# Performance work log

Measured on AMD Instinct MI355X. Metric: run time of the kernel, lower is better.

Reference implementation:

```python
import jax, jax.numpy as jnp
import numpy as np

EMBED_DIM = 1024
NUM_HEADS = 16
HEAD_DIM = EMBED_DIM // NUM_HEADS


def setup_inputs() -> dict:
    key = jax.random.key(0)
    ks = jax.random.split(key, 11)
    B, L, E = 4, 1024, EMBED_DIM
    s = E ** -0.5  # xavier-ish init scale
    return {
        "query": jax.random.normal(ks[0], (B, L, E), dtype=jnp.float32),
        "key": jax.random.normal(ks[1], (B, L, E), dtype=jnp.float32),
        "value": jax.random.normal(ks[2], (B, L, E), dtype=jnp.float32),
        "Wq": jax.random.normal(ks[3], (E, E), dtype=jnp.float32) * s,
        "bq": jnp.zeros((E,), dtype=jnp.float32),
        "Wk": jax.random.normal(ks[4], (E, E), dtype=jnp.float32) * s,
        "bk": jnp.zeros((E,), dtype=jnp.float32),
        "Wv": jax.random.normal(ks[5], (E, E), dtype=jnp.float32) * s,
        "bv": jnp.zeros((E,), dtype=jnp.float32),
        "Wo": jax.random.normal(ks[6], (E, E), dtype=jnp.float32) * s,
        "bo": jnp.zeros((E,), dtype=jnp.float32),
    }


def reference(query, key, value, Wq, bq, Wk, bk, Wv, bv, Wo, bo):
    # torch nn.MultiheadAttention (batch_first=True), need_weights=True,
    # average_attn_weights=False, eval mode (dropout inactive), no masks,
    # followed by the wrapper's extra softmax on the returned weights.
    B, Lq, E = query.shape
    Lk = key.shape[1]
    H, Dh = NUM_HEADS, HEAD_DIM
    scale = Dh ** -0.5

    # projections -> [B, H, L, Dh]
    q = (query @ Wq.T + bq).reshape(B, Lq, H, Dh).transpose(0, 2, 1, 3) * scale
    k = (key @ Wk.T + bk).reshape(B, Lk, H, Dh).transpose(0, 2, 1, 3)
    v = (value @ Wv.T + bv).reshape(B, Lk, H, Dh).transpose(0, 2, 1, 3)

    scores = jnp.einsum("bhqd,bhkd->bhqk", q, k)      # [B, H, Lq, Lk]
    attn = jax.nn.softmax(scores, axis=-1)             # attention weights

    ctx = jnp.einsum("bhqk,bhkd->bhqd", attn, v)       # [B, H, Lq, Dh]
    ctx = ctx.transpose(0, 2, 1, 3).reshape(B, Lq, E)
    out = ctx @ Wo.T + bo                              # [B, Lq, E]

    weights = jax.nn.softmax(attn, axis=-1)            # wrapper's redundant softmax
    return (out, weights)
```

## Files before the change

### kernel.cpp

```cpp
#include <hip/hip_runtime.h>
#include <cstdint>
#include <cstddef>

typedef short bf16x8 __attribute__((ext_vector_type(8)));
typedef float f32x4 __attribute__((ext_vector_type(4)));
typedef int v4i __attribute__((ext_vector_type(4)));
typedef unsigned short u16;

#define DEVFN static __device__ __forceinline__

#define M2 11.5415603f

DEVFN u16 f2bf(float f) {
  uint32_t u = __float_as_uint(f);
  u += 0x7FFFu + ((u >> 16) & 1u);
  return (u16)(u >> 16);
}

DEVFN f32x4 mfma16(bf16x8 a, bf16x8 b, f32x4 c) {
  return __builtin_amdgcn_mfma_f32_16x16x32_bf16(a, b, c, 0, 0, 0);
}

struct CvtArgs {
  const float* src[7];
  u16* dst[7];
  int n4[7];
};

__global__ __launch_bounds__(256) void cvt_all(CvtArgs a) {
  const int w = blockIdx.y;
  const int n4 = a.n4[w];
  const float4* s = (const float4*)a.src[w];
  uint2* d = (uint2*)a.dst[w];
  for (int i = blockIdx.x * 256 + threadIdx.x; i < n4; i += gridDim.x * 256) {
    const float4 v = s[i];
    d[i] = make_uint2((uint32_t)f2bf(v.x) | ((uint32_t)f2bf(v.y) << 16),
                      (uint32_t)f2bf(v.z) | ((uint32_t)f2bf(v.w) << 16));
  }
}

struct ProjArgs {
  const u16* A[3];
  const u16* W[3];
  const float* bias[3];
  u16* C[3];
  float scale[3];
};

__global__ __launch_bounds__(256) void gemm_proj(ProjArgs P) {
  constexpr int KD = 1024;
  constexpr int ND = 1024;
  __shared__ __align__(16) u16 As[128 * 32];
  __shared__ __align__(16) u16 Bs[128 * 32];
  const int hw = blockIdx.x + 32 * (blockIdx.y + 8 * blockIdx.z);
  const int lb = (hw & 7) * 96 + (hw >> 3);
  const int bn = lb & 7;
  const int bm = (lb >> 3) & 31;
  const int z  = lb >> 8;
  const u16* __restrict__ A = P.A[z];
  const u16* __restrict__ W = P.W[z];
  const float* __restrict__ bias = P.bias[z];
  u16* __restrict__ C = P.C[z];
  const float scale = P.scale[z];

  const int tid = threadIdx.x;
  const int wave = tid >> 6, lane = tid & 63;
  const int wm = wave >> 1, wn = wave & 1;
  const int l16 = lane & 15, lg = lane >> 4;

  f32x4 acc[4][4] = {};
  const int ar = wave * 16 + (lane >> 2);
  const int ac = (lane & 3) * 8;

  for (int k0 = 0; k0 < KD; k0 += 32) {
#pragma unroll
    for (int half = 0; half < 2; half++) {
      const int r = ar + half * 64;
      const u16* ga = A + (size_t)(bm * 128 + r) * KD + k0 + ac;
      const u16* gb = W + (size_t)(bn * 128 + r) * KD + k0 + ac;
      __builtin_amdgcn_global_load_lds(
          (const __attribute__((address_space(1))) void*)ga,
          (__attribute__((address_space(3))) void*)(As + wave * 512 + half * 2048),
          16, 0, 0);
      __builtin_amdgcn_global_load_lds(
          (const __attribute__((address_space(1))) void*)gb,
          (__attribute__((address_space(3))) void*)(Bs + wave * 512 + half * 2048),
          16, 0, 0);
    }
    __syncthreads();
    bf16x8 af[4], bfv[4];
#pragma unroll
    for (int m = 0; m < 4; m++)
      af[m] = *(const bf16x8*)(&As[(wm * 64 + m * 16 + l16) * 32 + lg * 8]);
#pragma unroll
    for (int n = 0; n < 4; n++)
      bfv[n] = *(const bf16x8*)(&Bs[(wn * 64 + n * 16 + l16) * 32 + lg * 8]);
#pragma unroll
    for (int m = 0; m < 4; m++)
#pragma unroll
      for (int n = 0; n < 4; n++)
        acc[m][n] = mfma16(af[m], bfv[n], acc[m][n]);
    __syncthreads();
  }

  if (z == 2) {
#pragma unroll
    for (int m = 0; m < 4; m++) {
#pragma unroll
      for (int n = 0; n < 4; n++) {
        const int col = bn * 128 + wn * 64 + n * 16 + l16;
        const float bv = bias[col];
        const int hh = col >> 6, dd = col & 63;
        const int row0 = bm * 128 + wm * 64 + m * 16 + lg * 4;
        const int bb = row0 >> 10, ll = row0 & 1023;
        u16 tmp[4];
#pragma unroll
        for (int r = 0; r < 4; r++) tmp[r] = f2bf((acc[m][n][r] + bv) * scale);
        *(uint2*)(C + ((size_t)((bb * 16 + hh) * 64 + dd)) * 1024 + ll) =
            *(const uint2*)tmp;
      }
    }
  } else {
#pragma unroll
    for (int m = 0; m < 4; m++) {
#pragma unroll
      for (int n = 0; n < 4; n++) {
        const int col = bn * 128 + wn * 64 + n * 16 + l16;
        const float bv = bias[col];
#pragma unroll
        for (int r = 0; r < 4; r++) {
          const int row = bm * 128 + wm * 64 + m * 16 + lg * 4 + r;
          C[(size_t)row * ND + col] = f2bf((acc[m][n][r] + bv) * scale);
        }
      }
    }
  }
}

__global__ __launch_bounds__(256) void gemm_out(const u16* __restrict__ A,
                                                const u16* __restrict__ W,
                                                const float* __restrict__ bias,
                                                float* __restrict__ C) {
  constexpr int KD = 1024;
  constexpr int ND = 1024;
  __shared__ __align__(16) u16 As[128 * 32];
  __shared__ __align__(16) u16 Bs[64 * 32];
  const int hw = blockIdx.x + 32 * blockIdx.y;
  const int lb = (hw & 7) * 64 + (hw >> 3);
  const int bn = lb & 15;
  const int bm = lb >> 4;
  const int tid = threadIdx.x;
  const int wave = tid >> 6, lane = tid & 63;
  const int wm = wave >> 1, wn = wave & 1;
  const int l16 = lane & 15, lg = lane >> 4;

  f32x4 acc[4][2] = {};
  const int ar = wave * 16 + (lane >> 2);
  const int ac = (lane & 3) * 8;

  for (int k0 = 0; k0 < KD; k0 += 32) {
#pragma unroll
    for (int half = 0; half < 2; half++) {
      const u16* ga = A + (size_t)(bm * 128 + ar + half * 64) * KD + k0 + ac;
      __builtin_amdgcn_global_load_lds(
          (const __attribute__((address_space(1))) void*)ga,
          (__attribute__((address_space(3))) void*)(As + wave * 512 + half * 2048),
          16, 0, 0);
    }
    {
      const u16* gb = W + (size_t)(bn * 64 + ar) * KD + k0 + ac;
      __builtin_amdgcn_global_load_lds(
          (const __attribute__((address_space(1))) void*)gb,
          (__attribute__((address_space(3))) void*)(Bs + wave * 512),
          16, 0, 0);
    }
    __syncthreads();
    bf16x8 af[4], bfv[2];
#pragma unroll
    for (int m = 0; m < 4; m++)
      af[m] = *(const bf16x8*)(&As[(wm * 64 + m * 16 + l16) * 32 + lg * 8]);
#pragma unroll
    for (int n = 0; n < 2; n++)
      bfv[n] = *(const bf16x8*)(&Bs[(wn * 32 + n * 16 + l16) * 32 + lg * 8]);
#pragma unroll
    for (int m = 0; m < 4; m++)
#pragma unroll
      for (int n = 0; n < 2; n++)
        acc[m][n] = mfma16(af[m], bfv[n], acc[m][n]);
    __syncthreads();
  }

#pragma unroll
  for (int m = 0; m < 4; m++) {
#pragma unroll
    for (int n = 0; n < 2; n++) {
      const int col = bn * 64 + wn * 32 + n * 16 + l16;
      const float bv = bias[col];
#pragma unroll
      for (int r = 0; r < 4; r++) {
        const int row = bm * 128 + wm * 64 + m * 16 + lg * 4 + r;
        C[(size_t)row * ND + col] = acc[m][n][r] + bv;
      }
    }
  }
}

__global__ __launch_bounds__(512, 4) void flash_kernel(
    const u16* __restrict__ Qs, const u16* __restrict__ Kb,
    const u16* __restrict__ Vt, u16* __restrict__ Ctx,
    float* __restrict__ Wout) {
  __shared__ __align__(16) u16 Ks[128 * 72];
  __shared__ __align__(16) u16 Vs[64 * 136];
  __shared__ __align__(16) u16 Ps[8][16 * 136];
  const int hw = blockIdx.x + 8 * (blockIdx.y + 16 * blockIdx.z);
  const int lb = (hw & 7) * 64 + (hw >> 3);
  const int qt = lb & 7;
  const int h  = (lb >> 3) & 15;
  const int b  = lb >> 7;
  const int tid = threadIdx.x, wave = tid >> 6, lane = tid & 63;
  const int l16 = lane & 15, lg = lane >> 4;
  const int bh = b * 16 + h;
  const int qbase = qt * 128 + wave * 16;

  const u16* qp = Qs + ((size_t)(b * 1024 + qbase + l16)) * 1024 + h * 64 + lg * 8;
  const bf16x8 qa0 = *(const bf16x8*)qp;
  const bf16x8 qa1 = *(const bf16x8*)(qp + 32);

  const int krow = tid >> 3, kcol = (tid & 7) * 8;
  const int vrow = tid >> 3, vcol = (tid & 7) * 16;
  const u16* kgb = Kb + ((size_t)(b * 1024 + krow)) * 1024 + h * 64 + kcol;
  const u16* vgb = Vt + ((size_t)(bh * 64 + vrow)) * 1024 + vcol;
  u16* kds = &Ks[krow * 72 + kcol];
  u16* vds = &Vs[vrow * 136 + vcol];

  v4i kpre[2], vpre[2];
#define LOADK(K0)                                                         \
  {                                                                       \
    _Pragma("unroll") for (int i_ = 0; i_ < 2; i_++)                      \
        kpre[i_] = *(const v4i*)(kgb + ((size_t)(K0) + i_ * 64) * 1024);  \
  }
#define LOADV(K0)                                                         \
  {                                                                       \
    _Pragma("unroll") for (int i_ = 0; i_ < 2; i_++)                      \
        vpre[i_] = *(const v4i*)(vgb + (size_t)(K0) + i_ * 8);            \
  }
#define WRITEK                                                            \
  {                                                                       \
    _Pragma("unroll") for (int i_ = 0; i_ < 2; i_++)                      \
        *(v4i*)(kds + i_ * 64 * 72) = kpre[i_];                           \
  }
#define WRITEV                                                            \
  {                                                                       \
    _Pragma("unroll") for (int i_ = 0; i_ < 2; i_++)                      \
        *(v4i*)(vds + i_ * 8) = vpre[i_];                                 \
  }

  float lsum[4] = {}, m2[4] = {};
  f32x4 o[4] = {};

  LOADK(0) LOADV(0)
  WRITEK WRITEV
  __syncthreads();

  for (int t = 0; t < 8; t++) {
    if (t < 7) { LOADK((t + 1) * 128) LOADV((t + 1) * 128) }

    u16* pw = &Ps[wave][0];
#pragma unroll
    for (int j = 0; j < 8; j++) {
      const u16* kr = &Ks[(j * 16 + l16) * 72 + lg * 8];
      const bf16x8 kf0 = *(const bf16x8*)kr;
      const bf16x8 kf1 = *(const bf16x8*)(kr + 32);
      f32x4 z = {0.f, 0.f, 0.f, 0.f};
      z = mfma16(qa0, kf0, z);
      z = mfma16(qa1, kf1, z);
#pragma unroll
      for (int r = 0; r < 4; r++) {
        const float p = __builtin_amdgcn_exp2f(z[r] - M2);
        lsum[r] += p;
        m2[r] += p * p;
        pw[(lg * 4 + r) * 136 + j * 16 + l16] = f2bf(p);
      }
    }

    bf16x8 pa[4];
#pragma unroll
    for (int ks = 0; ks < 4; ks++)
      pa[ks] = *(const bf16x8*)(&pw[l16 * 136 + ks * 32 + lg * 8]);
#pragma unroll
    for (int ds = 0; ds < 4; ds++) {
#pragma unroll
      for (int ks = 0; ks < 4; ks++) {
        const bf16x8 vb = *(const bf16x8*)(&Vs[(ds * 16 + l16) * 136 + ks * 32 + lg * 8]);
        o[ds] = mfma16(pa[ks], vb, o[ds]);
      }
    }
    __syncthreads();
    if (t < 7) { WRITEK WRITEV __syncthreads(); }
  }

  LOADK(0)

#pragma unroll
  for (int r = 0; r < 4; r++) {
#pragma unroll
    for (int sft = 1; sft < 16; sft <<= 1) {
      lsum[r] += __shfl_xor(lsum[r], sft);
      m2[r] += __shfl_xor(m2[r], sft);
    }
  }

  float il_[4], inv2_[4];
#pragma unroll
  for (int r = 0; r < 4; r++) {
    const float il = 1.0f / lsum[r];
    il_[r] = il;
    const float s2 = 1025.0f + 0.5f * m2[r] * il * il;
    inv2_[r] = 1.0f / s2;
    const int qg = qbase + lg * 4 + r;
#pragma unroll
    for (int ds = 0; ds < 4; ds++)
      Ctx[((size_t)(b * 1024 + qg)) * 1024 + h * 64 + ds * 16 + l16] =
          f2bf(o[ds][r] * il);
  }

  float* wr = Wout + ((size_t)bh * 1024 + qbase + lg * 4) * 1024 + l16;
#define EMIT_TILE(K0)                                                     \
  {                                                                       \
    _Pragma("unroll") for (int j = 0; j < 8; j++) {                       \
      const u16* kr = &Ks[(j * 16 + l16) * 72 + lg * 8];                  \
      const bf16x8 kf0 = *(const bf16x8*)kr;                              \
      const bf16x8 kf1 = *(const bf16x8*)(kr + 32);                       \
      f32x4 z = {0.f, 0.f, 0.f, 0.f};                                     \
      z = mfma16(qa0, kf0, z);                                            \
      z = mfma16(qa1, kf1, z);                                            \
      _Pragma("unroll") for (int r = 0; r < 4; r++) {                     \
        const float a = __builtin_amdgcn_exp2f(z[r] - M2) * il_[r];       \
        float u = fmaf(a, 0.16666667f, 0.5f);                             \
        u = fmaf(a, u, 1.0f);                                             \
        u = fmaf(a, u, 1.0f);                                             \
        wr[(size_t)r * 1024 + (K0) + j * 16] = u * inv2_[r];              \
      }                                                                   \
    }                                                                     \
  }

  EMIT_TILE(896)
  __syncthreads();
  WRITEK
  __syncthreads();
  for (int t = 0; t < 7; t++) {
    if (t < 6) LOADK((t + 1) * 128)
    EMIT_TILE(t * 128)
    __syncthreads();
    if (t < 6) { WRITEK __syncthreads(); }
  }
#undef EMIT_TILE
#undef LOADK
#undef LOADV
#undef WRITEK
#undef WRITEV
}

extern "C" void kernel_launch(void* const* d_in, const int* in_sizes, int n_in,
                              void* d_out, int out_size, void* d_ws, size_t ws_size,
                              hipStream_t stream) {
  (void)in_sizes; (void)n_in; (void)out_size; (void)ws_size;
  const float* query = (const float*)d_in[0];
  const float* key   = (const float*)d_in[1];
  const float* value = (const float*)d_in[2];
  const float* Wq = (const float*)d_in[3];
  const float* bq = (const float*)d_in[4];
  const float* Wk = (const float*)d_in[5];
  const float* bk = (const float*)d_in[6];
  const float* Wv = (const float*)d_in[7];
  const float* bv = (const float*)d_in[8];
  const float* Wo = (const float*)d_in[9];
  const float* bo = (const float*)d_in[10];

  const size_t MB = 1ull << 20;
  char* w = (char*)d_ws;
  u16* xq  = (u16*)(w + 0 * MB);
  u16* xk  = (u16*)(w + 8 * MB);
  u16* xv  = (u16*)(w + 16 * MB);
  u16* wqb = (u16*)(w + 24 * MB);
  u16* wkb = (u16*)(w + 26 * MB);
  u16* wvb = (u16*)(w + 28 * MB);
  u16* wob = (u16*)(w + 30 * MB);
  u16* Qp  = (u16*)(w + 32 * MB);
  u16* Kp  = (u16*)(w + 40 * MB);
  u16* ctx = xq;

  float* Out = (float*)d_out;
  float* Wts = (float*)d_out + 4 * 1024 * 1024;
  u16* vt = (u16*)d_out;

  CvtArgs ca;
  ca.src[0] = query; ca.dst[0] = xq;  ca.n4[0] = 1048576;
  ca.src[1] = key;   ca.dst[1] = xk;  ca.n4[1] = 1048576;
  ca.src[2] = value; ca.dst[2] = xv;  ca.n4[2] = 1048576;
  ca.src[3] = Wq;    ca.dst[3] = wqb; ca.n4[3] = 262144;
  ca.src[4] = Wk;    ca.dst[4] = wkb; ca.n4[4] = 262144;
  ca.src[5] = Wv;    ca.dst[5] = wvb; ca.n4[5] = 262144;
  ca.src[6] = Wo;    ca.dst[6] = wob; ca.n4[6] = 262144;
  cvt_all<<<dim3(512, 7), 256, 0, stream>>>(ca);

  ProjArgs pa;
  pa.A[0] = xq; pa.W[0] = wqb; pa.bias[0] = bq; pa.C[0] = Qp;
  pa.scale[0] = 0.125f * 1.44269504f;
  pa.A[1] = xk; pa.W[1] = wkb; pa.bias[1] = bk; pa.C[1] = Kp; pa.scale[1] = 1.0f;
  pa.A[2] = xv; pa.W[2] = wvb; pa.bias[2] = bv; pa.C[2] = vt; pa.scale[2] = 1.0f;
  gemm_proj<<<dim3(32, 8, 3), 256, 0, stream>>>(pa);

  flash_kernel<<<dim3(8, 16, 4), 512, 0, stream>>>(Qp, Kp, vt, ctx, Wts);

  gemm_out<<<dim3(32, 16), 256, 0, stream>>>(ctx, wob, bo, Out);
}
```

Measured before the change: 171.2 us.

## Double K-tile depth in projection GEMM and XOR-swizzle LDS layout

The QKV projection GEMM now stages 64-wide K slices per iteration instead of 32, which halves the number of barrier pairs and loop iterations. Global-to-LDS copies place each 16-byte chunk at an XOR-swizzled column, and the fragment reads apply the matching swizzle, so LDS bank conflicts on the MFMA operand reads should drop. LDS use per block doubles, which may reduce occupancy, and the loop is still single-buffered with no overlap between loads and MFMAs.

```diff
diff --git a/kernel.cpp b/kernel.cpp
--- a/kernel.cpp
+++ b/kernel.cpp
@@ -50,8 +50,8 @@
 __global__ __launch_bounds__(256) void gemm_proj(ProjArgs P) {
   constexpr int KD = 1024;
   constexpr int ND = 1024;
-  __shared__ __align__(16) u16 As[128 * 32];
-  __shared__ __align__(16) u16 Bs[128 * 32];
+  __shared__ __align__(16) u16 As[128 * 64];
+  __shared__ __align__(16) u16 Bs[128 * 64];
   const int hw = blockIdx.x + 32 * (blockIdx.y + 8 * blockIdx.z);
   const int lb = (hw & 7) * 96 + (hw >> 3);
   const int bn = lb & 7;
@@ -69,37 +69,49 @@
   const int l16 = lane & 15, lg = lane >> 4;
 
   f32x4 acc[4][4] = {};
-  const int ar = wave * 16 + (lane >> 2);
-  const int ac = (lane & 3) * 8;
-
-  for (int k0 = 0; k0 < KD; k0 += 32) {
-#pragma unroll
-    for (int half = 0; half < 2; half++) {
-      const int r = ar + half * 64;
-      const u16* ga = A + (size_t)(bm * 128 + r) * KD + k0 + ac;
-      const u16* gb = W + (size_t)(bn * 128 + r) * KD + k0 + ac;
+  const int sr = wave * 8 + (lane >> 3);
+  const int scol = (((lane & 7) ^ (lane >> 3)) * 8);
+
+  for (int k0 = 0; k0 < KD; k0 += 64) {
+#pragma unroll
+    for (int q = 0; q < 4; q++) {
+      const int r = sr + q * 32;
+      const u16* ga = A + (size_t)(bm * 128 + r) * KD + k0 + scol;
+      const u16* gb = W + (size_t)(bn * 128 + r) * KD + k0 + scol;
       __builtin_amdgcn_global_load_lds(
           (const __attribute__((address_space(1))) void*)ga,
-          (__attribute__((address_space(3))) void*)(As + wave * 512 + half * 2048),
+          (__attribute__((address_space(3))) void*)(As + (wave * 8 + q * 32) * 64),
           16, 0, 0);
       __builtin_amdgcn_global_load_lds(
           (const __attribute__((address_space(1))) void*)gb,
-          (__attribute__((address_space(3))) void*)(Bs + wave * 512 + half * 2048),
+          (__attribute__((address_space(3))) void*)(Bs + (wave * 8 + q * 32) * 64),
           16, 0, 0);
     }
     __syncthreads();
-    bf16x8 af[4], bfv[4];
+    bf16x8 af[4][2], bfv[4][2];
+#pragma unroll
+    for (int m = 0; m < 4; m++) {
+      const int rm = wm * 64 + m * 16 + l16;
+      const int sw = (l16 & 7) << 3;
+#pragma unroll
+      for (int kk = 0; kk < 2; kk++)
+        af[m][kk] = *(const bf16x8*)(&As[rm * 64 + ((kk * 32 + lg * 8) ^ sw)]);
+    }
+#pragma unroll
+    for (int n = 0; n < 4; n++) {
+      const int rn = wn * 64 + n * 16 + l16;
+      const int sw = (l16 & 7) << 3;
+#pragma unroll
+      for (int kk = 0; kk < 2; kk++)
+        bfv[n][kk] = *(const bf16x8*)(&Bs[rn * 64 + ((kk * 32 + lg * 8) ^ sw)]);
+    }
 #pragma unroll
     for (int m = 0; m < 4; m++)
-      af[m] = *(const bf16x8*)(&As[(wm * 64 + m * 16 + l16) * 32 + lg * 8]);
-#pragma unroll
-    for (int n = 0; n < 4; n++)
-      bfv[n] = *(const bf16x8*)(&Bs[(wn * 64 + n * 16 + l16) * 32 + lg * 8]);
-#pragma unroll
-    for (int m = 0; m < 4; m++)
 #pragma unroll
       for (int n = 0; n < 4; n++)
-        acc[m][n] = mfma16(af[m], bfv[n], acc[m][n]);
+#pragma unroll
+        for (int kk = 0; kk < 2; kk++)
+          acc[m][n] = mfma16(af[m][kk], bfv[n][kk], acc[m][n]);
     __syncthreads();
   }
 
```

Result: no change. 170.6 us (-0.3%).
